# Kernel tuning notes

Measured on AMD Instinct MI355X. Metric: run time of the kernel, lower is better.

The kernel has to match this reference:

```python
import jax, jax.numpy as jnp
import numpy as np
from jax import lax

# Model dims (match init_kwargs)
B, CX, XS = 32, 3, 64          # batch, x_channels, x_size
CY, K, S, Z = 32, 10, 1, 256   # y_channels, kernel_size, stride, z_size
M = (XS - K) // S + 1          # y_size = 55
FEAT = CY * M * M              # flattened y feature size
DT, TAU_X, TAU_Y = 0.1, 1.0, 0.2
BETA_Y, BETA_Z = 3.0, 7.0
STEPS = 30                     # max_num_steps
DN = ('NCHW', 'OIHW', 'NCHW')


def setup_inputs() -> dict:
    key = jax.random.key(0)
    k1, k2, k3 = jax.random.split(key, 3)
    x = jax.random.normal(k1, (B, CX, XS, XS), dtype=jnp.float32)
    # conv/convT share this kernel (torch ties convT.weight = conv.weight)
    Kw = jax.random.normal(k2, (CY, CX, K, K), dtype=jnp.float32) / np.sqrt(CX * K * K)
    # xavier_normal_ for W [Z, FEAT]
    W = jax.random.normal(k3, (Z, FEAT), dtype=jnp.float32) * np.sqrt(2.0 / (Z + FEAT))
    return {"x": x, "Kw": Kw, "W": W}


def _step(x, y, Kw, W):
    # fc: z = W @ softmax_channels(beta_y * y).flatten  -> [B, Z]
    fy = jax.nn.softmax(BETA_Y * y, axis=1)                       # softmax over channel dim
    z = jnp.einsum('zf,bf->bz', W, fy.reshape(fy.shape[0], -1))
    # nonlin_z: softmax over z-slots (dim=-2 of [B,N,1] == N axis)
    fz = jax.nn.softmax(BETA_Z * z, axis=-1)
    top = jnp.einsum('zf,bz->bf', W, fz).reshape(-1, CY, M, M)    # fcT
    conv_x = lax.conv_general_dilated(x, Kw, (S, S), 'VALID', dimension_numbers=DN)
    y_inst = conv_x + top
    y = y + DT / TAU_Y * (-y + y_inst)
    # x_instant = convT(softmax_channels(y))  (no beta here, matching the torch code)
    x_inst = lax.conv_transpose(jax.nn.softmax(y, axis=1), Kw, (S, S), 'VALID',
                                dimension_numbers=DN, transpose_kernel=True)
    x = x + DT / TAU_X * (-x + x_inst)
    return x, y


def reference(x, Kw, W):
    y0 = jnp.zeros((x.shape[0], CY, M, M), dtype=x.dtype)

    def body(carry, _):
        xc, yc = carry
        return _step(xc, yc, Kw, W), None

    (xf, _), _ = lax.scan(body, (x, y0), None, length=STEPS)
    return xf
```

## Files before the change

### kernel.cpp

```cpp
#include <hip/hip_runtime.h>

#define K_B    32
#define K_CXC  3
#define K_XS   64
#define K_CY   32
#define K_M    55
#define K_Z    256
#define K_P    (K_M*K_M)
#define K_FEAT (K_CY*K_P)
#define K_XN   (K_CXC*K_XS*K_XS)
#define K_NSPLIT 55

typedef __attribute__((ext_vector_type(8))) short short8;
typedef __attribute__((ext_vector_type(4))) float f32x4;

__device__ __forceinline__ short f2bf(float f) {
    unsigned u = __builtin_bit_cast(unsigned, f);
    unsigned r = (u + 0x7FFFu + ((u >> 16) & 1u)) >> 16;
    return (short)r;
}

__global__ __launch_bounds__(256) void w_perm1(const float* __restrict__ W,
                                               short* __restrict__ Wbp) {
    int o = blockIdx.x*256 + threadIdx.x;
    int zi = o / 12100, c = o - zi*12100;
    int p = c >> 2, cyg = c & 3;
    const float* wp = W + (size_t)zi*K_FEAT + p;
    short8 v;
    #pragma unroll
    for (int j = 0; j < 8; ++j) v[j] = f2bf(wp[(size_t)(cyg*8 + j)*K_P]);
    *(short8*)(Wbp + (size_t)o*8) = v;
}

__global__ __launch_bounds__(256) void w_perm2(const float* __restrict__ W,
                                               short* __restrict__ Wg2p) {
    int F = blockIdx.x*256 + threadIdx.x;
    if (F >= K_FEAT) return;
    int zb = blockIdx.y;
    int cy = F & 31, p = F >> 5;
    short8 o;
    #pragma unroll
    for (int j = 0; j < 8; ++j)
        o[j] = f2bf(W[(size_t)(zb*8 + j)*K_FEAT + cy*K_P + p]);
    *(short8*)(Wg2p + ((size_t)zb*K_FEAT + F)*8) = o;
}

__global__ __launch_bounds__(256) void prep_frags(const float* __restrict__ Kw,
                                                  short* __restrict__ KfragT,
                                                  short* __restrict__ Kfrag2) {
    int e = blockIdx.x*256 + threadIdx.x;
    if (e < 6400) {
        int uv = e >> 6, l = e & 63;
        int u = uv / 10, v = uv - u*10;
        int lr = l & 15, lg = l >> 4;
        short8 o;
        #pragma unroll
        for (int j = 0; j < 8; ++j) {
            int cy = lg*8 + j;
            o[j] = (lr < 3) ? f2bf(Kw[cy*300 + lr*100 + (9-u)*10 + (9-v)]) : (short)0;
        }
        *(short8*)(KfragT + (size_t)e*8) = o;
    } else if (e < 6400 + 1920) {
        int e2 = e - 6400;
        int kn = e2 >> 6, l = e2 & 63;
        int ks = kn >> 1, nt = kn & 1;
        int lr = l & 15, lg = l >> 4;
        short8 o;
        #pragma unroll
        for (int j = 0; j < 8; ++j) {
            int k = ks*32 + lg*8 + j;
            int cx = k / 160, rem = k - cx*160;
            int u = rem >> 4, v = rem & 15;
            o[j] = (v < 10) ? f2bf(Kw[(lr + nt*16)*300 + cx*100 + u*10 + v]) : (short)0;
        }
        *(short8*)(Kfrag2 + (size_t)e2*8) = o;
    }
}

__global__ __launch_bounds__(256) void fyb_fill(short* __restrict__ fyb) {
    size_t i = ((size_t)blockIdx.x*256 + threadIdx.x) * 8;
    if (i >= (size_t)K_B*K_FEAT) return;
    short8 o = {0x3D00,0x3D00,0x3D00,0x3D00,0x3D00,0x3D00,0x3D00,0x3D00};
    *(short8*)(fyb + i) = o;
}

__global__ __launch_bounds__(256) void fused_A(const float* __restrict__ x,
                                               float* __restrict__ cxb,
                                               const short* __restrict__ Wbp,
                                               const short* __restrict__ fyb,
                                               float* __restrict__ zpart,
                                               const short* __restrict__ Kfrag2) {
    __shared__ __align__(16) short xcopy[14400];
    int bid = blockIdx.x;
    int t = threadIdx.x;
    if (bid < 512) {
        int b = bid >> 4, tile = bid & 15;
        int i0 = (tile >> 2) * 16, j0 = (tile & 3) * 16;
        const float* xb = x + (size_t)b*K_XN;
        for (int e = t; e < 1800; e += 256) {
            int s = e / 225, rem = e - s*225;
            int cx = rem / 75, r2 = rem - cx*75;
            int row = r2 / 3, i16 = r2 - row*3;
            int gr = i0 + row;
            int gc0 = j0 + i16*8 + s;
            const float* xp = xb + cx*4096 + gr*64;
            short8 o;
            #pragma unroll
            for (int j = 0; j < 8; ++j) {
                int gc = gc0 + j;
                float v = (gr < 64 && gc < 64) ? xp[gc] : 0.f;
                o[j] = f2bf(v);
            }
            *(short8*)(xcopy + (size_t)e*8) = o;
        }
        __syncthreads();
        int wid = t >> 6, l = t & 63, lr = l & 15, lg = l >> 4;
        f32x4 acc[4][2];
        #pragma unroll
        for (int r = 0; r < 4; ++r) { acc[r][0] = (f32x4){0,0,0,0}; acc[r][1] = (f32x4){0,0,0,0}; }
        #pragma unroll 3
        for (int ks = 0; ks < 15; ++ks) {
            short8 a0 = *(const short8*)(Kfrag2 + ((size_t)(ks*2+0)*64 + l)*8);
            short8 a1 = *(const short8*)(Kfrag2 + ((size_t)(ks*2+1)*64 + l)*8);
            int koff = ks*32 + lg*8;
            int cx = koff / 160, rem = koff - cx*160;
            int u = rem >> 4, v0 = rem & 15;
            int w = lr + v0;
            int abase = (w & 7)*225 + cx*75 + (w >> 3);
            #pragma unroll
            for (int r = 0; r < 4; ++r) {
                int xrow = wid*4 + r + u;
                short8 bf = *(const short8*)(xcopy + (size_t)(abase + xrow*3)*8);
                acc[r][0] = __builtin_amdgcn_mfma_f32_16x16x32_bf16(a0, bf, acc[r][0], 0, 0, 0);
                acc[r][1] = __builtin_amdgcn_mfma_f32_16x16x32_bf16(a1, bf, acc[r][1], 0, 0, 0);
            }
        }
        int jcol = j0 + lr;
        bool jv = jcol < 55;
        #pragma unroll
        for (int r = 0; r < 4; ++r) {
            int ir = i0 + wid*4 + r;
            if (ir >= 55 || !jv) continue;
            size_t base = (size_t)b*K_FEAT + (size_t)(ir*55 + jcol)*32 + lg*4;
            *(f32x4*)&cxb[base]      = acc[r][0];
            *(f32x4*)&cxb[base + 16] = acc[r][1];
        }
    } else {
        int g = bid - 512;
        int bx = g & 3, by = g >> 2;
        int wid = t >> 6, l = t & 63;
        int lr = l & 15, lg = l >> 4;
        int zi0 = bx*64 + wid*16;
        int k0  = by*1760;
        const short* Ap  = Wbp + (size_t)(zi0 + lr)*K_FEAT + k0 + lg*8;
        const short* Bp0 = fyb + (size_t)(lr)*K_FEAT      + k0 + lg*8;
        const short* Bp1 = fyb + (size_t)(16 + lr)*K_FEAT + k0 + lg*8;
        f32x4 acc0 = {0.f,0.f,0.f,0.f}, acc1 = {0.f,0.f,0.f,0.f};
        #pragma unroll 5
        for (int k = 0; k < 55; ++k) {
            short8 a  = *(const short8*)(Ap  + k*32);
            short8 b0 = *(const short8*)(Bp0 + k*32);
            short8 b1 = *(const short8*)(Bp1 + k*32);
            acc0 = __builtin_amdgcn_mfma_f32_16x16x32_bf16(a, b0, acc0, 0, 0, 0);
            acc1 = __builtin_amdgcn_mfma_f32_16x16x32_bf16(a, b1, acc1, 0, 0, 0);
        }
        float* zp = zpart + (size_t)by*8192;
        #pragma unroll
        for (int r = 0; r < 4; ++r) {
            zp[(lr)*K_Z    + zi0 + lg*4 + r] = acc0[r];
            zp[(16+lr)*K_Z + zi0 + lg*4 + r] = acc1[r];
        }
    }
}

__global__ __launch_bounds__(256) void fzk(const float* __restrict__ zpart,
                                           short* __restrict__ fzb) {
    __shared__ float sr[256];
    int b = blockIdx.x, t = threadIdx.x;
    float zv = 0.f;
    #pragma unroll 5
    for (int p = 0; p < K_NSPLIT; ++p) zv += zpart[(size_t)p*8192 + b*K_Z + t];
    float v = 7.0f * zv;
    sr[t] = v; __syncthreads();
    for (int off = 128; off > 0; off >>= 1) {
        if (t < off) sr[t] = fmaxf(sr[t], sr[t+off]);
        __syncthreads();
    }
    float m = sr[0];
    __syncthreads();
    float e = __expf(v - m);
    sr[t] = e; __syncthreads();
    for (int off = 128; off > 0; off >>= 1) {
        if (t < off) sr[t] += sr[t+off];
        __syncthreads();
    }
    float s = sr[0];
    fzb[b*K_Z + t] = f2bf(e / s);
}

__global__ __launch_bounds__(256) void gemm2_sm(const short* __restrict__ Wg2p,
                                                const short* __restrict__ fzb,
                                                const float* __restrict__ cxb,
                                                float* __restrict__ y,
                                                short* __restrict__ syb,
                                                short* __restrict__ fyb) {
    int t = threadIdx.x;
    int wid = t >> 6, l = t & 63;
    int lr = l & 15, lg = l >> 4;
    int f0 = blockIdx.x*128 + wid*32;
    int p = f0 >> 5;
    if (p >= K_P) return;
    const short* A0 = fzb + (size_t)(lr)*K_Z      + lg*8;
    const short* A1 = fzb + (size_t)(16 + lr)*K_Z + lg*8;
    short8 af0[8], af1[8];
    #pragma unroll
    for (int k = 0; k < 8; ++k) {
        af0[k] = *(const short8*)(A0 + k*32);
        af1[k] = *(const short8*)(A1 + k*32);
    }
    f32x4 acc[2][2] = {{{0.f,0.f,0.f,0.f},{0.f,0.f,0.f,0.f}},
                       {{0.f,0.f,0.f,0.f},{0.f,0.f,0.f,0.f}}};
    #pragma unroll
    for (int nt = 0; nt < 2; ++nt) {
        #pragma unroll
        for (int k = 0; k < 8; ++k) {
            const short* bp = Wg2p + ((size_t)(k*4 + lg)*K_FEAT + f0 + nt*16 + lr)*8;
            short8 b = *(const short8*)bp;
            acc[0][nt] = __builtin_amdgcn_mfma_f32_16x16x32_bf16(af0[k], b, acc[0][nt], 0, 0, 0);
            acc[1][nt] = __builtin_amdgcn_mfma_f32_16x16x32_bf16(af1[k], b, acc[1][nt], 0, 0, 0);
        }
    }
    #pragma unroll
    for (int mt = 0; mt < 2; ++mt) {
        #pragma unroll
        for (int r = 0; r < 4; ++r) {
            int bb = mt*16 + lg*4 + r;
            size_t i0a = (size_t)bb*K_FEAT + f0 + lr;
            size_t i1a = i0a + 16;
            float v0 = 0.5f*(y[i0a] + cxb[i0a] + acc[mt][0][r]);
            float v1 = 0.5f*(y[i1a] + cxb[i1a] + acc[mt][1][r]);
            float mx = fmaxf(v0, v1);
            #pragma unroll
            for (int m = 1; m <= 8; m <<= 1) mx = fmaxf(mx, __shfl_xor(mx, m));
            float d0 = v0 - mx, d1 = v1 - mx;
            float e10 = __expf(d0),      e11 = __expf(d1);
            float e30 = __expf(3.0f*d0), e31 = __expf(3.0f*d1);
            float s1 = e10 + e11, s3 = e30 + e31;
            #pragma unroll
            for (int m = 1; m <= 8; m <<= 1) { s1 += __shfl_xor(s1, m); s3 += __shfl_xor(s3, m); }
            float i1 = 1.0f/s1, i3 = 1.0f/s3;
            y[i0a] = v0; y[i1a] = v1;
            syb[i0a] = f2bf(e10*i1); syb[i1a] = f2bf(e11*i1);
            fyb[i0a] = f2bf(e30*i3); fyb[i1a] = f2bf(e31*i3);
        }
    }
}

__global__ __launch_bounds__(256) void convT_mfma(const short* __restrict__ syb,
                                                  const short* __restrict__ KfragT,
                                                  float* __restrict__ x) {
    __shared__ __align__(16) short syt[25*41*32];
    int t = threadIdx.x;
    int tile = blockIdx.x;
    int b = blockIdx.y;
    int p0 = (tile >> 1) * 16, q0 = (tile & 1) * 32;
    for (int e = t; e < 1025; e += 256) {
        int row = e / 41, col = e - row*41;
        int gr = p0 - 9 + row, gc = q0 - 9 + col;
        short8 z = {0,0,0,0,0,0,0,0};
        short8 v0 = z, v1 = z, v2 = z, v3 = z;
        if (gr >= 0 && gr < 55 && gc >= 0 && gc < 55) {
            const short* sp = syb + ((size_t)b*K_P + gr*55 + gc) * 32;
            v0 = *(const short8*)(sp);
            v1 = *(const short8*)(sp + 8);
            v2 = *(const short8*)(sp + 16);
            v3 = *(const short8*)(sp + 24);
        }
        short* dp = syt + (size_t)e * 32;
        *(short8*)(dp)      = v0;
        *(short8*)(dp + 8)  = v1;
        *(short8*)(dp + 16) = v2;
        *(short8*)(dp + 24) = v3;
    }
    __syncthreads();
    int wid = t >> 6, l = t & 63, lr = l & 15, lg = l >> 4;
    f32x4 acc[4][2];
    #pragma unroll
    for (int r = 0; r < 4; ++r) { acc[r][0] = (f32x4){0,0,0,0}; acc[r][1] = (f32x4){0,0,0,0}; }
    const short* kfp = KfragT + (size_t)l * 8;
    for (int u = 0; u < 10; ++u) {
        #pragma unroll 5
        for (int v = 0; v < 10; ++v) {
            short8 a = *(const short8*)(kfp + (size_t)(u*10 + v)*512);
            #pragma unroll
            for (int r = 0; r < 4; ++r) {
                int rowlds = wid*4 + r + u;
                const short* bp = syt + ((size_t)(rowlds*41 + v + lr)*32 + lg*8);
                short8 b0 = *(const short8*)bp;
                short8 b1 = *(const short8*)(bp + 16*32);
                acc[r][0] = __builtin_amdgcn_mfma_f32_16x16x32_bf16(a, b0, acc[r][0], 0, 0, 0);
                acc[r][1] = __builtin_amdgcn_mfma_f32_16x16x32_bf16(a, b1, acc[r][1], 0, 0, 0);
            }
        }
    }
    if (lg == 0) {
        #pragma unroll
        for (int r = 0; r < 4; ++r) {
            int p = p0 + wid*4 + r;
            #pragma unroll
            for (int ct = 0; ct < 2; ++ct) {
                int q = q0 + ct*16 + lr;
                #pragma unroll
                for (int c = 0; c < 3; ++c) {
                    float* xp = x + (size_t)b*K_XN + c*4096 + p*64 + q;
                    *xp = 0.9f*(*xp) + 0.1f*acc[r][ct][c];
                }
            }
        }
    }
}

extern "C" void kernel_launch(void* const* d_in, const int* in_sizes, int n_in,
                              void* d_out, int out_size, void* d_ws, size_t ws_size,
                              hipStream_t stream) {
    const float* xin = (const float*)d_in[0];
    const float* Kw  = (const float*)d_in[1];
    const float* W   = (const float*)d_in[2];
    float* x = (float*)d_out;

    float* ws     = (float*)d_ws;
    float* y      = ws;
    float* cxb    = y     + 3097600;
    float* zpart  = cxb   + 3097600;
    short* fyb    = (short*)(zpart + 450560);
    short* fzb    = fyb   + 3097600;
    short* Wbp    = fzb   + 8192;
    short* Wg2p   = Wbp   + 24780800;
    short* syb    = Wg2p  + 24780800;
    short* KfragT = syb   + 3097600;
    short* Kfrag2 = KfragT+ 51200;

    hipMemcpyAsync(x, xin, (size_t)K_B*K_XN*sizeof(float), hipMemcpyDeviceToDevice, stream);
    hipMemsetAsync(y, 0, (size_t)3097600*sizeof(float), stream);
    prep_frags<<<33, 256, 0, stream>>>(Kw, KfragT, Kfrag2);
    w_perm1<<<12100, 256, 0, stream>>>(W, Wbp);
    w_perm2<<<dim3(379,32), 256, 0, stream>>>(W, Wg2p);
    fyb_fill<<<1513, 256, 0, stream>>>(fyb);

    for (int s = 0; s < 30; ++s) {
        fused_A<<<732, 256, 0, stream>>>(x, cxb, Wbp, fyb, zpart, Kfrag2);
        fzk<<<32, 256, 0, stream>>>(zpart, fzb);
        gemm2_sm<<<757, 256, 0, stream>>>(Wg2p, fzb, cxb, y, syb, fyb);
        convT_mfma<<<dim3(8,32), 256, 0, stream>>>(syb, KfragT, x);
    }
}
```

Baseline: 2.829 ms.

## Specialize first iteration analytically and restructure W permutation kernels

Since y starts at zero, the first step's channel softmax is uniform, so z for step one equals the row sums of W divided by the channel count. That sum is now computed during the W permutation, and a dedicated first-iteration path replaces the first GEMM with a single-block softmax, skipping the y memset and the fyb fill. The W permutation kernels are rewritten to use coalesced reads with an LDS transpose. The conv tile load is staged through shared float memory with float4 loads. The cost is extra kernels, an atomic reduction for the row sums, and more shared memory per block in fused_A.

```diff
diff --git a/kernel.cpp b/kernel.cpp
--- a/kernel.cpp
+++ b/kernel.cpp
@@ -20,29 +20,54 @@
     return (short)r;
 }
 
-__global__ __launch_bounds__(256) void w_perm1(const float* __restrict__ W,
-                                               short* __restrict__ Wbp) {
-    int o = blockIdx.x*256 + threadIdx.x;
-    int zi = o / 12100, c = o - zi*12100;
-    int p = c >> 2, cyg = c & 3;
-    const float* wp = W + (size_t)zi*K_FEAT + p;
-    short8 v;
-    #pragma unroll
-    for (int j = 0; j < 8; ++j) v[j] = f2bf(wp[(size_t)(cyg*8 + j)*K_P]);
-    *(short8*)(Wbp + (size_t)o*8) = v;
-}
-
-__global__ __launch_bounds__(256) void w_perm2(const float* __restrict__ W,
-                                               short* __restrict__ Wg2p) {
-    int F = blockIdx.x*256 + threadIdx.x;
-    if (F >= K_FEAT) return;
-    int zb = blockIdx.y;
-    int cy = F & 31, p = F >> 5;
-    short8 o;
-    #pragma unroll
-    for (int j = 0; j < 8; ++j)
-        o[j] = f2bf(W[(size_t)(zb*8 + j)*K_FEAT + cy*K_P + p]);
-    *(short8*)(Wg2p + ((size_t)zb*K_FEAT + F)*8) = o;
+__global__ __launch_bounds__(256) void w_perm1_t(const float* __restrict__ W,
+                                                 short* __restrict__ Wbp,
+                                                 float* __restrict__ zrow) {
+    __shared__ short ldt[256*33];
+    int t = threadIdx.x;
+    int pt = blockIdx.x, zi = blockIdx.y;
+    int p = pt*256 + t;
+    bool pv = p < K_P;
+    const float* wz = W + (size_t)zi*K_FEAT;
+    float sum = 0.f;
+    #pragma unroll 8
+    for (int cy = 0; cy < 32; ++cy) {
+        float v = pv ? wz[cy*K_P + p] : 0.f;
+        sum += v;
+        ldt[t*33 + cy] = f2bf(v);
+    }
+    #pragma unroll
+    for (int m = 1; m < 64; m <<= 1) sum += __shfl_xor(sum, m);
+    if ((t & 63) == 0) atomicAdd(&zrow[zi], sum);
+    __syncthreads();
+    if (pv) {
+        short8 o[4];
+        #pragma unroll
+        for (int g = 0; g < 4; ++g)
+            #pragma unroll
+            for (int j = 0; j < 8; ++j) o[g][j] = ldt[t*33 + g*8 + j];
+        short* dp = Wbp + (size_t)zi*K_FEAT + (size_t)p*32;
+        *(short8*)(dp)      = o[0];
+        *(short8*)(dp + 8)  = o[1];
+        *(short8*)(dp + 16) = o[2];
+        *(short8*)(dp + 24) = o[3];
+    }
+}
+
+__global__ __launch_bounds__(256) void w_perm2_r(const float* __restrict__ W,
+                                                 short* __restrict__ Wg2p) {
+    int t = threadIdx.x;
+    int pt = blockIdx.x, zb = blockIdx.y;
+    int p = pt*256 + t;
+    if (p >= K_P) return;
+    #pragma unroll 4
+    for (int cy = 0; cy < 32; ++cy) {
+        short8 o;
+        #pragma unroll
+        for (int j = 0; j < 8; ++j)
+            o[j] = f2bf(W[(size_t)(zb*8 + j)*K_FEAT + cy*K_P + p]);
+        *(short8*)(Wg2p + ((size_t)zb*K_FEAT + (size_t)p*32 + cy)*8) = o;
+    }
 }
 
 __global__ __launch_bounds__(256) void prep_frags(const float* __restrict__ Kw,
@@ -77,11 +102,64 @@
     }
 }
 
-__global__ __launch_bounds__(256) void fyb_fill(short* __restrict__ fyb) {
-    size_t i = ((size_t)blockIdx.x*256 + threadIdx.x) * 8;
-    if (i >= (size_t)K_B*K_FEAT) return;
-    short8 o = {0x3D00,0x3D00,0x3D00,0x3D00,0x3D00,0x3D00,0x3D00,0x3D00};
-    *(short8*)(fyb + i) = o;
+__device__ __forceinline__ void conv_body(const float* __restrict__ x,
+                                          float* __restrict__ cxb,
+                                          const short* __restrict__ Kfrag2,
+                                          int b, int tile, int t,
+                                          short* xcopy, float* xraw) {
+    int i0 = (tile >> 2) * 16, j0 = (tile & 3) * 16;
+    const float* xb = x + (size_t)b*K_XN;
+    for (int e = t; e < 600; e += 256) {
+        int rowid = e >> 3, q = e & 7;
+        int cx = rowid / 25, rr = rowid - cx*25;
+        int gr = i0 + rr, gc = j0 + q*4;
+        float4 v = {0.f,0.f,0.f,0.f};
+        if (gr < 64 && gc < 64) v = *(const float4*)(xb + cx*4096 + gr*64 + gc);
+        *(float4*)&xraw[(cx*25+rr)*32 + q*4] = v;
+    }
+    __syncthreads();
+    for (int e = t; e < 1800; e += 256) {
+        int s = e / 225, rem = e - s*225;
+        int cx = rem / 75, r2 = rem - cx*75;
+        int row = r2 / 3, i16 = r2 - row*3;
+        const float* rp = &xraw[(cx*25+row)*32 + i16*8 + s];
+        short8 o;
+        #pragma unroll
+        for (int j = 0; j < 8; ++j) o[j] = f2bf(rp[j]);
+        *(short8*)(xcopy + (size_t)e*8) = o;
+    }
+    __syncthreads();
+    int wid = t >> 6, l = t & 63, lr = l & 15, lg = l >> 4;
+    f32x4 acc[4][2];
+    #pragma unroll
+    for (int r = 0; r < 4; ++r) { acc[r][0] = (f32x4){0,0,0,0}; acc[r][1] = (f32x4){0,0,0,0}; }
+    #pragma unroll 3
+    for (int ks = 0; ks < 15; ++ks) {
+        short8 a0 = *(const short8*)(Kfrag2 + ((size_t)(ks*2+0)*64 + l)*8);
+        short8 a1 = *(const short8*)(Kfrag2 + ((size_t)(ks*2+1)*64 + l)*8);
+        int koff = ks*32 + lg*8;
+        int cx = koff / 160, rem = koff - cx*160;
+        int u = rem >> 4, v0 = rem & 15;
+        int w = lr + v0;
+        int abase = (w & 7)*225 + cx*75 + (w >> 3);
+        #pragma unroll
+        for (int r = 0; r < 4; ++r) {
+            int xrow = wid*4 + r + u;
+            short8 bf = *(const short8*)(xcopy + (size_t)(abase + xrow*3)*8);
+            acc[r][0] = __builtin_amdgcn_mfma_f32_16x16x32_bf16(a0, bf, acc[r][0], 0, 0, 0);
+            acc[r][1] = __builtin_amdgcn_mfma_f32_16x16x32_bf16(a1, bf, acc[r][1], 0, 0, 0);
+        }
+    }
+    int jcol = j0 + lr;
+    bool jv = jcol < 55;
+    #pragma unroll
+    for (int r = 0; r < 4; ++r) {
+        int ir = i0 + wid*4 + r;
+        if (ir >= 55 || !jv) continue;
+        size_t base = (size_t)b*K_FEAT + (size_t)(ir*55 + jcol)*32 + lg*4;
+        *(f32x4*)&cxb[base]      = acc[r][0];
+        *(f32x4*)&cxb[base + 16] = acc[r][1];
+    }
 }
 
 __global__ __launch_bounds__(256) void fused_A(const float* __restrict__ x,
@@ -91,60 +169,11 @@
                                                float* __restrict__ zpart,
                                                const short* __restrict__ Kfrag2) {
     __shared__ __align__(16) short xcopy[14400];
+    __shared__ __align__(16) float xraw[2400];
     int bid = blockIdx.x;
     int t = threadIdx.x;
     if (bid < 512) {
-        int b = bid >> 4, tile = bid & 15;
-        int i0 = (tile >> 2) * 16, j0 = (tile & 3) * 16;
-        const float* xb = x + (size_t)b*K_XN;
-        for (int e = t; e < 1800; e += 256) {
-            int s = e / 225, rem = e - s*225;
-            int cx = rem / 75, r2 = rem - cx*75;
-            int row = r2 / 3, i16 = r2 - row*3;
-            int gr = i0 + row;
-            int gc0 = j0 + i16*8 + s;
-            const float* xp = xb + cx*4096 + gr*64;
-            short8 o;
-            #pragma unroll
-            for (int j = 0; j < 8; ++j) {
-                int gc = gc0 + j;
-                float v = (gr < 64 && gc < 64) ? xp[gc] : 0.f;
-                o[j] = f2bf(v);
-            }
-            *(short8*)(xcopy + (size_t)e*8) = o;
-        }
-        __syncthreads();
-        int wid = t >> 6, l = t & 63, lr = l & 15, lg = l >> 4;
-        f32x4 acc[4][2];
-        #pragma unroll
-        for (int r = 0; r < 4; ++r) { acc[r][0] = (f32x4){0,0,0,0}; acc[r][1] = (f32x4){0,0,0,0}; }
-        #pragma unroll 3
-        for (int ks = 0; ks < 15; ++ks) {
-            short8 a0 = *(const short8*)(Kfrag2 + ((size_t)(ks*2+0)*64 + l)*8);
-            short8 a1 = *(const short8*)(Kfrag2 + ((size_t)(ks*2+1)*64 + l)*8);
-            int koff = ks*32 + lg*8;
-            int cx = koff / 160, rem = koff - cx*160;
-            int u = rem >> 4, v0 = rem & 15;
-            int w = lr + v0;
-            int abase = (w & 7)*225 + cx*75 + (w >> 3);
-            #pragma unroll
-            for (int r = 0; r < 4; ++r) {
-                int xrow = wid*4 + r + u;
-                short8 bf = *(const short8*)(xcopy + (size_t)(abase + xrow*3)*8);
-                acc[r][0] = __builtin_amdgcn_mfma_f32_16x16x32_bf16(a0, bf, acc[r][0], 0, 0, 0);
-                acc[r][1] = __builtin_amdgcn_mfma_f32_16x16x32_bf16(a1, bf, acc[r][1], 0, 0, 0);
-            }
-        }
-        int jcol = j0 + lr;
-        bool jv = jcol < 55;
-        #pragma unroll
-        for (int r = 0; r < 4; ++r) {
-            int ir = i0 + wid*4 + r;
-            if (ir >= 55 || !jv) continue;
-            size_t base = (size_t)b*K_FEAT + (size_t)(ir*55 + jcol)*32 + lg*4;
-            *(f32x4*)&cxb[base]      = acc[r][0];
-            *(f32x4*)&cxb[base + 16] = acc[r][1];
-        }
+        conv_body(x, cxb, Kfrag2, bid >> 4, bid & 15, t, xcopy, xraw);
     } else {
         int g = bid - 512;
         int bx = g & 3, by = g >> 2;
@@ -173,6 +202,15 @@
     }
 }
 
+__global__ __launch_bounds__(256) void conv_first(const float* __restrict__ x,
+                                                  float* __restrict__ cxb,
+                                                  const short* __restrict__ Kfrag2) {
+    __shared__ __align__(16) short xcopy[14400];
+    __shared__ __align__(16) float xraw[2400];
+    int bid = blockIdx.x;
+    conv_body(x, cxb, Kfrag2, bid >> 4, bid & 15, threadIdx.x, xcopy, xraw);
+}
+
 __global__ __launch_bounds__(256) void fzk(const float* __restrict__ zpart,
                                            short* __restrict__ fzb) {
     __shared__ float sr[256];
@@ -198,6 +236,31 @@
     fzb[b*K_Z + t] = f2bf(e / s);
 }
 
+__global__ __launch_bounds__(256) void fzk_first(const float* __restrict__ zrow,
+                                                 short* __restrict__ fzb) {
+    __shared__ float sr[256];
+    int t = threadIdx.x;
+    float v = 7.0f * zrow[t] * 0.03125f;
+    sr[t] = v; __syncthreads();
+    for (int off = 128; off > 0; off >>= 1) {
+        if (t < off) sr[t] = fmaxf(sr[t], sr[t+off]);
+        __syncthreads();
+    }
+    float m = sr[0];
+    __syncthreads();
+    float e = __expf(v - m);
+    sr[t] = e; __syncthreads();
+    for (int off = 128; off > 0; off >>= 1) {
+        if (t < off) sr[t] += sr[t+off];
+        __syncthreads();
+    }
+    float s = sr[0];
+    short r = f2bf(e / s);
+    #pragma unroll
+    for (int b = 0; b < 32; ++b) fzb[b*K_Z + t] = r;
+}
+
+template<bool FIRST>
 __global__ __launch_bounds__(256) void gemm2_sm(const short* __restrict__ Wg2p,
                                                 const short* __restrict__ fzb,
                                                 const float* __restrict__ cxb,
@@ -208,8 +271,7 @@
     int wid = t >> 6, l = t & 63;
     int lr = l & 15, lg = l >> 4;
     int f0 = blockIdx.x*128 + wid*32;
-    int p = f0 >> 5;
-    if (p >= K_P) return;
+    if (f0 >= K_FEAT) return;
     const short* A0 = fzb + (size_t)(lr)*K_Z      + lg*8;
     const short* A1 = fzb + (size_t)(16 + lr)*K_Z + lg*8;
     short8 af0[8], af1[8];
@@ -237,8 +299,14 @@
             int bb = mt*16 + lg*4 + r;
             size_t i0a = (size_t)bb*K_FEAT + f0 + lr;
             size_t i1a = i0a + 16;
-            float v0 = 0.5f*(y[i0a] + cxb[i0a] + acc[mt][0][r]);
-            float v1 = 0.5f*(y[i1a] + cxb[i1a] + acc[mt][1][r]);
+            float v0, v1;
+            if (FIRST) {
+                v0 = 0.5f*(cxb[i0a] + acc[mt][0][r]);
+                v1 = 0.5f*(cxb[i1a] + acc[mt][1][r]);
+            } else {
+                v0 = 0.5f*(y[i0a] + cxb[i0a] + acc[mt][0][r]);
+                v1 = 0.5f*(y[i1a] + cxb[i1a] + acc[mt][1][r]);
+            }
             float mx = fmaxf(v0, v1);
             #pragma unroll
             for (int m = 1; m <= 8; m <<= 1) mx = fmaxf(mx, __shfl_xor(mx, m));
@@ -332,7 +400,8 @@
     float* y      = ws;
     float* cxb    = y     + 3097600;
     float* zpart  = cxb   + 3097600;
-    short* fyb    = (short*)(zpart + 450560);
+    float* zrow   = zpart + 450560;
+    short* fyb    = (short*)(zrow + 256);
     short* fzb    = fyb   + 3097600;
     short* Wbp    = fzb   + 8192;
     short* Wg2p   = Wbp   + 24780800;
@@ -341,16 +410,20 @@
     short* Kfrag2 = KfragT+ 51200;
 
     hipMemcpyAsync(x, xin, (size_t)K_B*K_XN*sizeof(float), hipMemcpyDeviceToDevice, stream);
-    hipMemsetAsync(y, 0, (size_t)3097600*sizeof(float), stream);
+    hipMemsetAsync(zrow, 0, 256*sizeof(float), stream);
     prep_frags<<<33, 256, 0, stream>>>(Kw, KfragT, Kfrag2);
-    w_perm1<<<12100, 256, 0, stream>>>(W, Wbp);
-    w_perm2<<<dim3(379,32), 256, 0, stream>>>(W, Wg2p);
-    fyb_fill<<<1513, 256, 0, stream>>>(fyb);
-
-    for (int s = 0; s < 30; ++s) {
+    w_perm1_t<<<dim3(12,256), 256, 0, stream>>>(W, Wbp, zrow);
+    w_perm2_r<<<dim3(12,32), 256, 0, stream>>>(W, Wg2p);
+
+    conv_first<<<512, 256, 0, stream>>>(x, cxb, Kfrag2);
+    fzk_first<<<1, 256, 0, stream>>>(zrow, fzb);
+    gemm2_sm<true><<<757, 256, 0, stream>>>(Wg2p, fzb, cxb, y, syb, fyb);
+    convT_mfma<<<dim3(8,32), 256, 0, stream>>>(syb, KfragT, x);
+
+    for (int s = 1; s < 30; ++s) {
         fused_A<<<732, 256, 0, stream>>>(x, cxb, Wbp, fyb, zpart, Kfrag2);
         fzk<<<32, 256, 0, stream>>>(zpart, fzb);
-        gemm2_sm<<<757, 256, 0, stream>>>(Wg2p, fzb, cxb, y, syb, fyb);
+        gemm2_sm<false><<<757, 256, 0, stream>>>(Wg2p, fzb, cxb, y, syb, fyb);
         convT_mfma<<<dim3(8,32), 256, 0, stream>>>(syb, KfragT, x);
     }
 }
```

Measured after the change: 2.664 ms. 1.06x faster.
